# Kernel tuning notes

Measured on AMD Instinct MI355X. Metric: run time of the kernel, lower is better.

## Reference

```python
import jax, jax.numpy as jnp
import numpy as np

B, N, T_OBS, N_HEAD, D = 4, 2048, 8, 4, 16  # D = t_obs*2 = in/out feat of GAT
S, NSAMP = 2, 20
OUT_DIM = S * NSAMP  # 40
SEG = 64  # pedestrians per scene -> 32 scenes, block-diagonal mask


def _xavier(key, shape, gain=1.414):
    fan_in, fan_out = shape[-2], shape[-1]
    a = gain * np.sqrt(6.0 / (fan_in + fan_out))
    return jax.random.uniform(key, shape, jnp.float32, -a, a)


def setup_inputs() -> dict:
    key = jax.random.key(0)
    ks = jax.random.split(key, 12)
    x = jax.random.normal(ks[0], (B, N, T_OBS, 2), jnp.float32)
    # block-diagonal scene mask: 32 scenes of 64 peds each
    scene_id = jnp.arange(N) // SEG
    mask = (scene_id[:, None] == scene_id[None, :]).astype(jnp.float32)
    w = _xavier(ks[1], (N_HEAD, D, D))
    a_src = _xavier(ks[2], (N_HEAD, D, 1))
    a_dst = _xavier(ks[3], (N_HEAD, D, 1))
    bias = jnp.zeros((D,), jnp.float32)
    # MLP dims: (16,) + (16, 64) + (40,)
    W1 = _xavier(ks[4], (D, 16), gain=1.0)
    b1 = jnp.zeros((16,), jnp.float32)
    W2 = _xavier(ks[5], (16, 64), gain=1.0)
    b2 = jnp.zeros((64,), jnp.float32)
    W3 = _xavier(ks[6], (64, OUT_DIM), gain=1.0)
    b3 = jnp.zeros((OUT_DIM,), jnp.float32)
    return {"x": x, "mask": mask, "w": w, "a_src": a_src, "a_dst": a_dst,
            "bias": bias, "W1": W1, "b1": b1, "W2": W2, "b2": b2, "W3": W3, "b3": b3}


def reference(x, mask, w, a_src, a_dst, bias, W1, b1, W2, b2, W3, b3):
    b, n = x.shape[0], x.shape[1]
    node = x.reshape(b, n, -1)                       # (B, N, 16)
    # GAT
    hp = jnp.einsum('bni,hio->bhno', node, w)        # (B, H, N, D)
    attn_src = jnp.einsum('bhno,hoe->bhne', hp, a_src)[..., 0]  # (B, H, N)
    attn_dst = jnp.einsum('bhno,hoe->bhne', hp, a_dst)[..., 0]  # (B, H, N)
    attn = attn_src[:, :, :, None] * attn_dst[:, :, None, :]    # (B, H, N, N)
    attn = jnp.where(attn >= 0, attn, 0.2 * attn)    # leaky_relu(0.2)
    attn = jax.nn.softmax(attn, axis=-1)             # softmax over full row
    attn = attn * mask                                # mask AFTER softmax (as in source)
    out = jnp.einsum('bhnm,bhmo->bno', attn, hp) + bias
    out = out + hp.sum(axis=1)                        # skip connection
    # MLP head: activation applied BEFORE each Linear (per source), dropout disabled
    y = jax.nn.relu(out) @ W1 + b1
    y = jax.nn.relu(y) @ W2 + b2
    y = jax.nn.relu(y) @ W3 + b3
    y = y.reshape(b, n, NSAMP, -1)[..., 0:S]          # (B, N, 20, 2)
    return jnp.clip(jax.nn.sigmoid(y), 0.01, 0.99)
```

## Files before the change

### kernel.cpp

```cpp
#include <hip/hip_runtime.h>
#include <math.h>

#define NB 4
#define NN 2048
#define NH 4
#define ND 16
#define SEG 64

__global__ __launch_bounds__(256) void k_proj(
    const float* __restrict__ x, const float* __restrict__ w,
    const float* __restrict__ a_src, const float* __restrict__ a_dst,
    float* __restrict__ hp, float* __restrict__ src, float* __restrict__ dst)
{
    __shared__ float w_s[ND * ND];
    __shared__ float as_s[ND], ad_s[ND];
    int t = threadIdx.x;
    int b = blockIdx.x >> 5;
    int h = (blockIdx.x >> 3) & 3;
    w_s[t] = w[h * 256 + t];
    if (t < 16) { as_s[t] = a_src[h * 16 + t]; ad_s[t] = a_dst[h * 16 + t]; }
    __syncthreads();

    int idx = blockIdx.x * 256 + t;
    int n = idx & 2047;

    const float4* xp = (const float4*)(x + (size_t)(b * NN + n) * ND);
    float4 x0 = xp[0], x1 = xp[1], x2 = xp[2], x3 = xp[3];
    float nv[16];
    nv[0]=x0.x; nv[1]=x0.y; nv[2]=x0.z; nv[3]=x0.w;
    nv[4]=x1.x; nv[5]=x1.y; nv[6]=x1.z; nv[7]=x1.w;
    nv[8]=x2.x; nv[9]=x2.y; nv[10]=x2.z; nv[11]=x2.w;
    nv[12]=x3.x; nv[13]=x3.y; nv[14]=x3.z; nv[15]=x3.w;

    float acc[16];
    #pragma unroll
    for (int o = 0; o < 16; ++o) acc[o] = 0.f;
    #pragma unroll
    for (int i = 0; i < 16; ++i) {
        float ni = nv[i];
        #pragma unroll
        for (int o = 0; o < 16; ++o) acc[o] = fmaf(ni, w_s[i * 16 + o], acc[o]);
    }
    float sv = 0.f, dv = 0.f;
    #pragma unroll
    for (int o = 0; o < 16; ++o) {
        sv = fmaf(acc[o], as_s[o], sv);
        dv = fmaf(acc[o], ad_s[o], dv);
    }
    float4* hpp = (float4*)(hp + (size_t)idx * 16);
    hpp[0] = make_float4(acc[0],  acc[1],  acc[2],  acc[3]);
    hpp[1] = make_float4(acc[4],  acc[5],  acc[6],  acc[7]);
    hpp[2] = make_float4(acc[8],  acc[9],  acc[10], acc[11]);
    hpp[3] = make_float4(acc[12], acc[13], acc[14], acc[15]);
    src[idx] = sv;
    dst[idx] = dv;
}

__global__ __launch_bounds__(256) void k_denom(
    const float* __restrict__ src, const float* __restrict__ dst,
    float* __restrict__ maxe, float* __restrict__ denom)
{
    __shared__ __align__(16) float d_s[NN];
    __shared__ float rmax[4], rmin[4];
    int t = threadIdx.x;
    int bh   = blockIdx.x >> 6;
    int tile = blockIdx.x & 63;

    const float4* dsrc4 = (const float4*)(dst + (size_t)bh * NN);
    float4* d4s = (float4*)d_s;
    float mx = -3.4e38f, mn = 3.4e38f;
    #pragma unroll
    for (int u = 0; u < 2; ++u) {
        float4 v = dsrc4[t + u * 256];
        d4s[t + u * 256] = v;
        mx = fmaxf(mx, fmaxf(fmaxf(v.x, v.y), fmaxf(v.z, v.w)));
        mn = fminf(mn, fminf(fminf(v.x, v.y), fminf(v.z, v.w)));
    }
    #pragma unroll
    for (int off = 32; off >= 1; off >>= 1) {
        mx = fmaxf(mx, __shfl_xor(mx, off));
        mn = fminf(mn, __shfl_xor(mn, off));
    }
    if ((t & 63) == 0) { rmax[t >> 6] = mx; rmin[t >> 6] = mn; }
    __syncthreads();
    float dmax = fmaxf(fmaxf(rmax[0], rmax[1]), fmaxf(rmax[2], rmax[3]));
    float dmin = fminf(fminf(rmin[0], rmin[1]), fminf(rmin[2], rmin[3]));

    int row = t >> 3, o = t & 7;
    int r = tile * 32 + row;
    float s  = src[(size_t)bh * NN + r];
    float sel = (s >= 0.f) ? dmax : dmin;
    float me  = s * sel;
    me = fmaxf(me, 0.2f * me);
    float s2  = 0.2f * s;
    float nme = -me;

    float a0 = 0.f, a1 = 0.f, a2 = 0.f, a3 = 0.f;
    #pragma unroll 8
    for (int j = 0; j < 64; ++j) {
        float4 dv = d4s[o + (j << 3)];
        float e0 = fmaxf(fmaf(s, dv.x, nme), fmaf(s2, dv.x, nme)); a0 += __expf(e0);
        float e1 = fmaxf(fmaf(s, dv.y, nme), fmaf(s2, dv.y, nme)); a1 += __expf(e1);
        float e2 = fmaxf(fmaf(s, dv.z, nme), fmaf(s2, dv.z, nme)); a2 += __expf(e2);
        float e3 = fmaxf(fmaf(s, dv.w, nme), fmaf(s2, dv.w, nme)); a3 += __expf(e3);
    }
    float acc = (a0 + a1) + (a2 + a3);
    #pragma unroll
    for (int off = 4; off >= 1; off >>= 1) acc += __shfl_xor(acc, off);
    if (o == 0) {
        denom[(size_t)bh * NN + r] = acc;
        maxe [(size_t)bh * NN + r] = me;
    }
}

__global__ __launch_bounds__(256) void k_scene(
    const float* __restrict__ hp, const float* __restrict__ src,
    const float* __restrict__ dst, const float* __restrict__ maxe,
    const float* __restrict__ denom, const float* __restrict__ bias,
    const float* __restrict__ W1, const float* __restrict__ b1,
    const float* __restrict__ W2, const float* __restrict__ b2,
    const float* __restrict__ W3, const float* __restrict__ b3,
    float* __restrict__ out)
{
    __shared__ __align__(16) float hp_s[NH][SEG][16];
    __shared__ float d_s[NH][SEG];
    __shared__ __align__(16) float po[NH][32][16];
    __shared__ float feat[32][17];
    __shared__ float y1s[32][17];
    __shared__ float y2s[32][65];
    __shared__ __align__(16) float w1s[256];
    __shared__ __align__(16) float w2s[1024];
    __shared__ float w3s[2560];
    __shared__ float b0s[16], b1s[16], b2s[64], b3s[40];

    int t    = threadIdx.x;
    int b    = blockIdx.x >> 6;
    int sc   = (blockIdx.x >> 1) & 31;
    int half = blockIdx.x & 1;
    int n0 = sc * SEG;
    int r0 = n0 + half * 32;

    for (int u = t; u < 1024; u += 256) {
        int h = u >> 8, rem = u & 255;
        ((float4*)hp_s)[u] =
            ((const float4*)(hp + ((size_t)(b * 4 + h) * NN + n0) * 16))[rem];
    }
    {
        int h = t >> 6, m = t & 63;
        d_s[h][m] = dst[(size_t)(b * 4 + h) * NN + n0 + m];
    }
    w1s[t] = W1[t];
    for (int u = t; u < 1024; u += 256) w2s[u] = W2[u];
    for (int u = t; u < 2560; u += 256) w3s[u] = W3[u];
    if (t < 16) { b0s[t] = bias[t]; b1s[t] = b1[t]; }
    if (t < 64) b2s[t] = b2[t];
    if (t < 40) b3s[t] = b3[t];
    __syncthreads();

    {
        int h = t >> 6, lane = t & 63;
        int nn = lane >> 1, p = lane & 1;
        size_t base = (size_t)(b * 4 + h) * NN + r0 + nn;
        float s   = src[base];
        float me  = maxe[base];
        float inv = 1.f / denom[base];
        float s2  = 0.2f * s;
        float nme = -me;
        float a[16];
        #pragma unroll
        for (int i = 0; i < 16; ++i) a[i] = 0.f;
        int m0 = p * 32;
        #pragma unroll 4
        for (int mm = 0; mm < 32; ++mm) {
            int m = m0 + mm;
            float dvv = d_s[h][m];
            float e = fmaxf(fmaf(s, dvv, nme), fmaf(s2, dvv, nme));
            float pr = __expf(e) * inv;
            const float* hr = &hp_s[h][m][0];
            #pragma unroll
            for (int i = 0; i < 16; ++i) a[i] = fmaf(pr, hr[i], a[i]);
        }
        #pragma unroll
        for (int i = 0; i < 16; ++i) a[i] += __shfl_xor(a[i], 1);
        if (p == 0) {
            #pragma unroll
            for (int i = 0; i < 16; ++i) po[h][nn][i] = a[i];
        }
    }
    __syncthreads();

    {
        int nn = t >> 3, q = t & 7;
        #pragma unroll
        for (int j = 0; j < 2; ++j) {
            int i = q * 2 + j;
            float v = b0s[i];
            #pragma unroll
            for (int h = 0; h < 4; ++h)
                v += po[h][nn][i] + hp_s[h][half * 32 + nn][i];
            feat[nn][i] = v;
        }
    }
    __syncthreads();

    {
        int nn = t >> 3, q = t & 7;
        float acc0 = b1s[q * 2], acc1 = b1s[q * 2 + 1];
        #pragma unroll
        for (int i = 0; i < 16; ++i) {
            float r = fmaxf(feat[nn][i], 0.f);
            acc0 = fmaf(r, w1s[i * 16 + q * 2],     acc0);
            acc1 = fmaf(r, w1s[i * 16 + q * 2 + 1], acc1);
        }
        y1s[nn][q * 2]     = acc0;
        y1s[nn][q * 2 + 1] = acc1;
    }
    __syncthreads();

    {
        int nn = t >> 3, q = t & 7;
        float acc[8];
        #pragma unroll
        for (int c = 0; c < 8; ++c) acc[c] = b2s[q * 8 + c];
        #pragma unroll
        for (int j = 0; j < 16; ++j) {
            float r = fmaxf(y1s[nn][j], 0.f);
            #pragma unroll
            for (int c = 0; c < 8; ++c)
                acc[c] = fmaf(r, w2s[j * 64 + q * 8 + c], acc[c]);
        }
        #pragma unroll
        for (int c = 0; c < 8; ++c) y2s[nn][q * 8 + c] = acc[c];
    }
    __syncthreads();

    {
        int nn = t >> 3, q = t & 7;
        float acc[5];
        #pragma unroll
        for (int c = 0; c < 5; ++c) acc[c] = b3s[q * 5 + c];
        #pragma unroll 8
        for (int k = 0; k < 64; ++k) {
            float r = fmaxf(y2s[nn][k], 0.f);
            #pragma unroll
            for (int c = 0; c < 5; ++c)
                acc[c] = fmaf(r, w3s[k * 40 + q * 5 + c], acc[c]);
        }
        float* op = out + ((size_t)(b * NN + r0 + nn) * 40) + q * 5;
        #pragma unroll
        for (int c = 0; c < 5; ++c) {
            float v = 1.f / (1.f + __expf(-acc[c]));
            v = fminf(fmaxf(v, 0.01f), 0.99f);
            op[c] = v;
        }
    }
}

extern "C" void kernel_launch(void* const* d_in, const int* in_sizes, int n_in,
                              void* d_out, int out_size, void* d_ws, size_t ws_size,
                              hipStream_t stream) {
    (void)in_sizes; (void)n_in; (void)out_size; (void)ws_size;
    const float* x     = (const float*)d_in[0];
    const float* w     = (const float*)d_in[2];
    const float* a_src = (const float*)d_in[3];
    const float* a_dst = (const float*)d_in[4];
    const float* bias  = (const float*)d_in[5];
    const float* W1    = (const float*)d_in[6];
    const float* b1    = (const float*)d_in[7];
    const float* W2    = (const float*)d_in[8];
    const float* b2    = (const float*)d_in[9];
    const float* W3    = (const float*)d_in[10];
    const float* b3    = (const float*)d_in[11];

    float* ws    = (float*)d_ws;
    float* hp    = ws;
    float* srcb  = hp + 524288;
    float* dstb  = srcb + 32768;
    float* maxe  = dstb + 32768;
    float* denom = maxe + 32768;
    float* outp  = (float*)d_out;

    hipLaunchKernelGGL(k_proj, dim3(128), dim3(256), 0, stream,
                       x, w, a_src, a_dst, hp, srcb, dstb);
    hipLaunchKernelGGL(k_denom, dim3(1024), dim3(256), 0, stream,
                       srcb, dstb, maxe, denom);
    hipLaunchKernelGGL(k_scene, dim3(256), dim3(256), 0, stream,
                       hp, srcb, dstb, maxe, denom, bias,
                       W1, b1, W2, b2, W3, b3, outp);
}
```

Before: 33.51 us.

## Split scene blocks into quarters, shrink proj blocks, use exp2 with prescaled logits

k_proj now runs 256 blocks of 128 threads, and k_scene runs 512 blocks that each handle 16 rows instead of 32. In the attention loop four lanes now share one row's 64 neighbours, and the MLP stages are remapped to 16 threads per row. Exponentials switch from __expf to exp2f with logits and the stored max prescaled by log2(e), which saves a multiply per exponent. The aim is more blocks on the many CUs for these small launches. The cost is that each k_scene block reloads the full scene hp and all MLP weights twice as often, and the third MLP stage leaves half its threads idle.

```diff
diff --git a/kernel.cpp b/kernel.cpp
--- a/kernel.cpp
+++ b/kernel.cpp
@@ -6,8 +6,9 @@
 #define NH 4
 #define ND 16
 #define SEG 64
-
-__global__ __launch_bounds__(256) void k_proj(
+#define L2E 1.4426950408889634f
+
+__global__ __launch_bounds__(128) void k_proj(
     const float* __restrict__ x, const float* __restrict__ w,
     const float* __restrict__ a_src, const float* __restrict__ a_dst,
     float* __restrict__ hp, float* __restrict__ src, float* __restrict__ dst)
@@ -15,14 +16,14 @@
     __shared__ float w_s[ND * ND];
     __shared__ float as_s[ND], ad_s[ND];
     int t = threadIdx.x;
-    int b = blockIdx.x >> 5;
-    int h = (blockIdx.x >> 3) & 3;
+    int idx = blockIdx.x * 128 + t;
+    int h = (idx >> 11) & 3;
+    int b = idx >> 13;
+    int n = idx & 2047;
     w_s[t] = w[h * 256 + t];
+    w_s[t + 128] = w[h * 256 + t + 128];
     if (t < 16) { as_s[t] = a_src[h * 16 + t]; ad_s[t] = a_dst[h * 16 + t]; }
     __syncthreads();
-
-    int idx = blockIdx.x * 256 + t;
-    int n = idx & 2047;
 
     const float4* xp = (const float4*)(x + (size_t)(b * NN + n) * ND);
     float4 x0 = xp[0], x1 = xp[1], x2 = xp[2], x3 = xp[3];
@@ -92,24 +93,25 @@
     float sel = (s >= 0.f) ? dmax : dmin;
     float me  = s * sel;
     me = fmaxf(me, 0.2f * me);
-    float s2  = 0.2f * s;
-    float nme = -me;
+    float sL  = s * L2E;
+    float s2L = 0.2f * sL;
+    float nme = -me * L2E;
 
     float a0 = 0.f, a1 = 0.f, a2 = 0.f, a3 = 0.f;
     #pragma unroll 8
     for (int j = 0; j < 64; ++j) {
         float4 dv = d4s[o + (j << 3)];
-        float e0 = fmaxf(fmaf(s, dv.x, nme), fmaf(s2, dv.x, nme)); a0 += __expf(e0);
-        float e1 = fmaxf(fmaf(s, dv.y, nme), fmaf(s2, dv.y, nme)); a1 += __expf(e1);
-        float e2 = fmaxf(fmaf(s, dv.z, nme), fmaf(s2, dv.z, nme)); a2 += __expf(e2);
-        float e3 = fmaxf(fmaf(s, dv.w, nme), fmaf(s2, dv.w, nme)); a3 += __expf(e3);
+        float e0 = fmaxf(fmaf(sL, dv.x, nme), fmaf(s2L, dv.x, nme)); a0 += exp2f(e0);
+        float e1 = fmaxf(fmaf(sL, dv.y, nme), fmaf(s2L, dv.y, nme)); a1 += exp2f(e1);
+        float e2 = fmaxf(fmaf(sL, dv.z, nme), fmaf(s2L, dv.z, nme)); a2 += exp2f(e2);
+        float e3 = fmaxf(fmaf(sL, dv.w, nme), fmaf(s2L, dv.w, nme)); a3 += exp2f(e3);
     }
     float acc = (a0 + a1) + (a2 + a3);
     #pragma unroll
     for (int off = 4; off >= 1; off >>= 1) acc += __shfl_xor(acc, off);
     if (o == 0) {
         denom[(size_t)bh * NN + r] = acc;
-        maxe [(size_t)bh * NN + r] = me;
+        maxe [(size_t)bh * NN + r] = me * L2E;
     }
 }
 
@@ -124,23 +126,25 @@
 {
     __shared__ __align__(16) float hp_s[NH][SEG][16];
     __shared__ float d_s[NH][SEG];
-    __shared__ __align__(16) float po[NH][32][16];
-    __shared__ float feat[32][17];
-    __shared__ float y1s[32][17];
-    __shared__ float y2s[32][65];
+    __shared__ __align__(16) float po[NH][16][16];
+    __shared__ float feat[16][17];
+    __shared__ float y1s[16][17];
+    __shared__ float y2s[16][65];
     __shared__ __align__(16) float w1s[256];
     __shared__ __align__(16) float w2s[1024];
     __shared__ float w3s[2560];
     __shared__ float b0s[16], b1s[16], b2s[64], b3s[40];
 
     int t    = threadIdx.x;
-    int b    = blockIdx.x >> 6;
-    int sc   = (blockIdx.x >> 1) & 31;
-    int half = blockIdx.x & 1;
+    int b    = blockIdx.x >> 7;
+    int sc   = (blockIdx.x >> 2) & 31;
+    int q4   = blockIdx.x & 3;
     int n0 = sc * SEG;
-    int r0 = n0 + half * 32;
-
-    for (int u = t; u < 1024; u += 256) {
+    int r0 = n0 + q4 * 16;
+
+    #pragma unroll
+    for (int k = 0; k < 4; ++k) {
+        int u = t + k * 256;
         int h = u >> 8, rem = u & 255;
         ((float4*)hp_s)[u] =
             ((const float4*)(hp + ((size_t)(b * 4 + h) * NN + n0) * 16))[rem];
@@ -159,29 +163,31 @@
 
     {
         int h = t >> 6, lane = t & 63;
-        int nn = lane >> 1, p = lane & 1;
+        int nn = lane >> 2, p = lane & 3;
         size_t base = (size_t)(b * 4 + h) * NN + r0 + nn;
-        float s   = src[base];
-        float me  = maxe[base];
+        float sL  = src[base] * L2E;
+        float s2L = 0.2f * sL;
+        float nme = -maxe[base];
         float inv = 1.f / denom[base];
-        float s2  = 0.2f * s;
-        float nme = -me;
         float a[16];
         #pragma unroll
         for (int i = 0; i < 16; ++i) a[i] = 0.f;
-        int m0 = p * 32;
+        int m0 = p * 16;
         #pragma unroll 4
-        for (int mm = 0; mm < 32; ++mm) {
+        for (int mm = 0; mm < 16; ++mm) {
             int m = m0 + mm;
             float dvv = d_s[h][m];
-            float e = fmaxf(fmaf(s, dvv, nme), fmaf(s2, dvv, nme));
-            float pr = __expf(e) * inv;
+            float e = fmaxf(fmaf(sL, dvv, nme), fmaf(s2L, dvv, nme));
+            float pr = exp2f(e) * inv;
             const float* hr = &hp_s[h][m][0];
             #pragma unroll
             for (int i = 0; i < 16; ++i) a[i] = fmaf(pr, hr[i], a[i]);
         }
         #pragma unroll
-        for (int i = 0; i < 16; ++i) a[i] += __shfl_xor(a[i], 1);
+        for (int i = 0; i < 16; ++i) {
+            a[i] += __shfl_xor(a[i], 1);
+            a[i] += __shfl_xor(a[i], 2);
+        }
         if (p == 0) {
             #pragma unroll
             for (int i = 0; i < 16; ++i) po[h][nn][i] = a[i];
@@ -190,68 +196,64 @@
     __syncthreads();
 
     {
-        int nn = t >> 3, q = t & 7;
-        #pragma unroll
-        for (int j = 0; j < 2; ++j) {
-            int i = q * 2 + j;
-            float v = b0s[i];
-            #pragma unroll
-            for (int h = 0; h < 4; ++h)
-                v += po[h][nn][i] + hp_s[h][half * 32 + nn][i];
-            feat[nn][i] = v;
-        }
-    }
-    __syncthreads();
-
-    {
-        int nn = t >> 3, q = t & 7;
-        float acc0 = b1s[q * 2], acc1 = b1s[q * 2 + 1];
+        int nn = t >> 4, i = t & 15;
+        float v = b0s[i];
+        #pragma unroll
+        for (int h = 0; h < 4; ++h)
+            v += po[h][nn][i] + hp_s[h][q4 * 16 + nn][i];
+        feat[nn][i] = v;
+    }
+    __syncthreads();
+
+    {
+        int nn = t >> 4, j = t & 15;
+        float acc = b1s[j];
         #pragma unroll
         for (int i = 0; i < 16; ++i) {
             float r = fmaxf(feat[nn][i], 0.f);
-            acc0 = fmaf(r, w1s[i * 16 + q * 2],     acc0);
-            acc1 = fmaf(r, w1s[i * 16 + q * 2 + 1], acc1);
-        }
-        y1s[nn][q * 2]     = acc0;
-        y1s[nn][q * 2 + 1] = acc1;
-    }
-    __syncthreads();
-
-    {
-        int nn = t >> 3, q = t & 7;
-        float acc[8];
-        #pragma unroll
-        for (int c = 0; c < 8; ++c) acc[c] = b2s[q * 8 + c];
+            acc = fmaf(r, w1s[i * 16 + j], acc);
+        }
+        y1s[nn][j] = acc;
+    }
+    __syncthreads();
+
+    {
+        int nn = t >> 4, g = t & 15;
+        float acc[4];
+        #pragma unroll
+        for (int c = 0; c < 4; ++c) acc[c] = b2s[g * 4 + c];
         #pragma unroll
         for (int j = 0; j < 16; ++j) {
             float r = fmaxf(y1s[nn][j], 0.f);
             #pragma unroll
-            for (int c = 0; c < 8; ++c)
-                acc[c] = fmaf(r, w2s[j * 64 + q * 8 + c], acc[c]);
-        }
-        #pragma unroll
-        for (int c = 0; c < 8; ++c) y2s[nn][q * 8 + c] = acc[c];
-    }
-    __syncthreads();
-
-    {
-        int nn = t >> 3, q = t & 7;
-        float acc[5];
-        #pragma unroll
-        for (int c = 0; c < 5; ++c) acc[c] = b3s[q * 5 + c];
-        #pragma unroll 8
-        for (int k = 0; k < 64; ++k) {
-            float r = fmaxf(y2s[nn][k], 0.f);
-            #pragma unroll
-            for (int c = 0; c < 5; ++c)
-                acc[c] = fmaf(r, w3s[k * 40 + q * 5 + c], acc[c]);
-        }
-        float* op = out + ((size_t)(b * NN + r0 + nn) * 40) + q * 5;
-        #pragma unroll
-        for (int c = 0; c < 5; ++c) {
-            float v = 1.f / (1.f + __expf(-acc[c]));
-            v = fminf(fmaxf(v, 0.01f), 0.99f);
-            op[c] = v;
+            for (int c = 0; c < 4; ++c)
+                acc[c] = fmaf(r, w2s[j * 64 + g * 4 + c], acc[c]);
+        }
+        #pragma unroll
+        for (int c = 0; c < 4; ++c) y2s[nn][g * 4 + c] = acc[c];
+    }
+    __syncthreads();
+
+    {
+        int nn = t >> 4, g = t & 15;
+        if (g < 8) {
+            float acc[5];
+            #pragma unroll
+            for (int c = 0; c < 5; ++c) acc[c] = b3s[g * 5 + c];
+            #pragma unroll 8
+            for (int k = 0; k < 64; ++k) {
+                float r = fmaxf(y2s[nn][k], 0.f);
+                #pragma unroll
+                for (int c = 0; c < 5; ++c)
+                    acc[c] = fmaf(r, w3s[k * 40 + g * 5 + c], acc[c]);
+            }
+            float* op = out + ((size_t)(b * NN + r0 + nn) * 40) + g * 5;
+            #pragma unroll
+            for (int c = 0; c < 5; ++c) {
+                float v = 1.f / (1.f + __expf(-acc[c]));
+                v = fminf(fmaxf(v, 0.01f), 0.99f);
+                op[c] = v;
+            }
         }
     }
 }
@@ -280,11 +282,11 @@
     float* denom = maxe + 32768;
     float* outp  = (float*)d_out;
 
-    hipLaunchKernelGGL(k_proj, dim3(128), dim3(256), 0, stream,
+    hipLaunchKernelGGL(k_proj, dim3(256), dim3(128), 0, stream,
                        x, w, a_src, a_dst, hp, srcb, dstb);
     hipLaunchKernelGGL(k_denom, dim3(1024), dim3(256), 0, stream,
                        srcb, dstb, maxe, denom);
-    hipLaunchKernelGGL(k_scene, dim3(256), dim3(256), 0, stream,
+    hipLaunchKernelGGL(k_scene, dim3(512), dim3(256), 0, stream,
                        hp, srcb, dstb, maxe, denom, bias,
                        W1, b1, W2, b2, W3, b3, outp);
 }
```

Measured after the change: 43.09 us. 1.29x slower.
